# Performance work log

Measured on AMD Instinct MI355X. Metric: run time of the kernel, lower is better.

The kernel has to match this reference:

```python
import jax, jax.numpy as jnp
import numpy as np
from jax import lax

# dims (match init_kwargs)
NC, BS, H, W, OC, NT = 4, 16, 64, 64, 12, 32


def _conv(x, w):
    # NHWC 'same' 3x3 conv
    return lax.conv_general_dilated(x, w, (1, 1), 'SAME',
                                    dimension_numbers=('NHWC', 'HWIO', 'NHWC'))


def _convlstm_step(x, h, c, Wx, Wh, b):
    # Keras ConvLSTM2D, single timestep. Gate order i, f, g(c), o; activation=tanh,
    # recurrent_activation=hard_sigmoid.
    z = _conv(x, Wx) + _conv(h, Wh) + b
    i, f, g, o = jnp.split(z, 4, axis=-1)
    i = jax.nn.hard_sigmoid(i)
    f = jax.nn.hard_sigmoid(f)
    o = jax.nn.hard_sigmoid(o)
    c_new = f * c + i * jnp.tanh(g)
    h_new = o * jnp.tanh(c_new)
    return h_new, c_new


def setup_inputs() -> dict:
    key = jax.random.key(0)
    ks = jax.random.split(key, 8)
    sc = lambda k, shp: jax.random.normal(k, shp, jnp.float32) * 0.05
    return {
        'x': jax.random.normal(ks[0], (BS, NT, H, W, OC), jnp.float32),
        'class_ids': jax.random.randint(ks[1], (NT,), 0, NC),
        'Wx_g': sc(ks[2], (3, 3, NC * OC, 4 * OC)),  # general cell input kernel
        'Wh_g': sc(ks[3], (3, 3, OC, 4 * OC)),       # general cell recurrent kernel
        'b_g': jnp.zeros((4 * OC,), jnp.float32),
        'Wx_c': sc(ks[4], (3, 3, 2 * OC, 4 * OC)),   # class cell input kernel
        'Wh_c': sc(ks[5], (3, 3, OC, 4 * OC)),       # class cell recurrent kernel
        'b_c': jnp.zeros((4 * OC,), jnp.float32),
    }


def reference(x, class_ids, Wx_g, Wh_g, b_g, Wx_c, Wh_c, b_c):
    def step(carry, inp):
        class_h, class_c, gen_h, gen_c = carry
        frame, cid = inp
        # general cell reads the whole class-state bank (raw reshape, as in TF source)
        x_gen = jnp.reshape(class_h, (BS, H, W, NC * OC))
        gen_h, gen_c = _convlstm_step(x_gen, gen_h, gen_c, Wx_g, Wh_g, b_g)
        # class cell reads frame + fresh general representation
        aug = jnp.concatenate([frame, gen_h], axis=-1)  # (BS,H,W,2*OC)
        h_new, c_new = _convlstm_step(aug, class_h[cid], class_c[cid], Wx_c, Wh_c, b_c)
        # scatter update into class-indexed state banks
        class_h = class_h.at[cid].set(h_new)
        class_c = class_c.at[cid].set(c_new)
        return (class_h, class_c, gen_h, gen_c), h_new.reshape(BS, -1)

    z = jnp.zeros((NC, BS, H, W, OC), jnp.float32)
    g = jnp.zeros((BS, H, W, OC), jnp.float32)
    xs = (jnp.swapaxes(x, 0, 1), class_ids)  # time-major
    _, outs = lax.scan(step, (z, z, g, g), xs)
    # OuterLayer: sum over time of flattened per-step outputs
    return jnp.sum(outs, axis=0)  # (BS, H*W*OC)
```

## Files before the change

### kernel.cpp

```cpp
#include <hip/hip_runtime.h>
#include <hip/hip_bf16.h>

#define NCLS 4
#define BS   16
#define NT   32
#define OC   12
#define HW   4096
#define PIX  65536
#define STATE 786432
#define BANK  3145728

typedef short bf16x8 __attribute__((ext_vector_type(8)));
typedef float f32x4  __attribute__((ext_vector_type(4)));

__device__ __forceinline__ float hsig(float v){
    return fminf(fmaxf((v + 3.0f) * (1.0f/6.0f), 0.0f), 1.0f);
}
__device__ __forceinline__ short f2bf(float f){
    union { __hip_bfloat16 h; short s; } u;
    u.h = __float2bfloat16(f);
    return u.s;
}

__global__ __launch_bounds__(256) void repack_kernel(
    const float* __restrict__ Wxg, const float* __restrict__ Whg,
    const float* __restrict__ Wxc, const float* __restrict__ Whc,
    bf16x8* __restrict__ wgt)
{
    int id = blockIdx.x * 256 + threadIdx.x;
    if (id >= 6912) return;
    int cell = id / 3456;
    int rem  = id - cell * 3456;
    int tap  = rem / 384;  rem -= tap * 384;
    int kb   = rem / 192;  rem -= kb * 192;
    int nt   = rem / 64;
    int lane = rem - nt * 64;
    int quad = lane >> 4;
    int n    = nt * 16 + (lane & 15);
    union { bf16x8 v; short s[8]; } o;
    #pragma unroll
    for (int j = 0; j < 8; ++j){
        int k = kb * 32 + quad * 8 + j;
        float f = 0.0f;
        if (cell == 0){
            if (k < 48)      f = Wxg[(tap*48 + k)*48 + n];
            else if (k < 60) f = Whg[(tap*12 + (k-48))*48 + n];
        } else {
            if (k < 24)      f = Wxc[(tap*24 + k)*48 + n];
            else if (k < 36) f = Whc[(tap*12 + (k-24))*48 + n];
        }
        o.s[j] = f2bf(f);
    }
    wgt[id] = o.v;
}

__global__ __launch_bounds__(256) void convert_kernel(
    const float* __restrict__ x, short* __restrict__ xbf)
{
    int i = blockIdx.x * 256 + threadIdx.x;
    const float4* xf = (const float4*)x;
    float4 a = xf[i*2], b = xf[i*2 + 1];
    union { bf16x8 v; short s[8]; } o;
    o.s[0]=f2bf(a.x); o.s[1]=f2bf(a.y); o.s[2]=f2bf(a.z); o.s[3]=f2bf(a.w);
    o.s[4]=f2bf(b.x); o.s[5]=f2bf(b.y); o.s[6]=f2bf(b.z); o.s[7]=f2bf(b.w);
    ((bf16x8*)xbf)[i] = o.v;
}

#define HALO_SHORTS (8*198*8)

__device__ __forceinline__ int row_swizzle(int bid){
    return ((bid & 7) << 7) | (bid >> 3);
}

__global__ __launch_bounds__(256) void gen_kernel(
    short* __restrict__ bank,
    const short* __restrict__ hin,
    short* __restrict__ hout,
    float* __restrict__ cstate,
    const short* __restrict__ htmp_prev,
    const int* __restrict__ ids, int t,
    const bf16x8* __restrict__ wgt,
    const float* __restrict__ bias)
{
    __shared__ __align__(16) short halo[HALO_SHORTS];
    const int tid = threadIdx.x;
    const int rb  = row_swizzle(blockIdx.x);
    const int p0  = rb << 6;
    const int b   = p0 >> 12;
    const int y   = (p0 >> 6) & 63;

    const int cprev = (t > 0) ? ids[t-1] : -1;
    const bool slotmatch = (cprev >= 0) && ((b >> 2) == cprev);
    const short* bsrc = slotmatch ? htmp_prev : bank;

    for (int tk = tid; tk < 1584; tk += 256){
        int rc = tk >> 3, q8 = tk & 7;
        int r  = rc / 66, c = rc - r * 66;
        int yy = y + r - 1, xx = c - 1;
        bool valid = (yy >= 0) & (yy < 64) & (xx >= 0) & (xx < 64);
        int p  = (b << 12) + (yy << 6) + xx;
        int pb = slotmatch ? (p & 16383) : p;
        union { bf16x8 v; uint2 u2[2]; uint4 u4; } ch;
        ch.u4 = make_uint4(0u, 0u, 0u, 0u);
        if (valid){
            if (q8 < 6){
                ch.u4 = *(const uint4*)(bsrc + pb*48 + q8*8);
                if (slotmatch && r == 1)
                    *(uint4*)(bank + p*48 + q8*8) = ch.u4;
            } else if (q8 == 6){
                ch.u2[0] = *(const uint2*)(hin + p*12);
                ch.u2[1] = *(const uint2*)(hin + p*12 + 4);
            } else {
                ch.u2[0] = *(const uint2*)(hin + p*12 + 8);
            }
        }
        *(bf16x8*)&halo[(q8*198 + rc)*8] = ch.v;
    }
    __syncthreads();

    const int lane = tid & 63;
    const int w    = tid >> 6;
    const int m    = lane & 15;
    const int quad = lane >> 4;
    const int colbase = 16*w + m;

    f32x4 acc0 = {0.f,0.f,0.f,0.f};
    f32x4 acc1 = acc0, acc2 = acc0;
    #pragma unroll
    for (int ky = 0; ky < 3; ++ky){
        #pragma unroll
        for (int kx = 0; kx < 3; ++kx){
            const int tap = ky*3 + kx;
            #pragma unroll
            for (int kb = 0; kb < 2; ++kb){
                const bf16x8 a = *(const bf16x8*)
                    &halo[(((kb*4 + quad)*198) + ky*66 + colbase + kx)*8];
                const bf16x8* wp = wgt + ((tap*2 + kb)*3)*64 + lane;
                acc0 = __builtin_amdgcn_mfma_f32_16x16x32_bf16(a, wp[0],   acc0, 0,0,0);
                acc1 = __builtin_amdgcn_mfma_f32_16x16x32_bf16(a, wp[64],  acc1, 0,0,0);
                acc2 = __builtin_amdgcn_mfma_f32_16x16x32_bf16(a, wp[128], acc2, 0,0,0);
            }
        }
    }

    __syncthreads();
    float* zw = ((float*)halo) + w * 768;
    #pragma unroll
    for (int r = 0; r < 4; ++r){
        zw[(quad*4 + r)*48 +      m] = acc0[r];
        zw[(quad*4 + r)*48 + 16 + m] = acc1[r];
        zw[(quad*4 + r)*48 + 32 + m] = acc2[r];
    }
    __syncthreads();
    const int pbase = p0 + 16*w;
    #pragma unroll
    for (int s = 0; s < 3; ++s){
        int idx = lane*3 + s;
        int px  = idx / 12;
        int j   = idx - px*12;
        float zi = zw[px*48 +      j] + bias[j];
        float zf = zw[px*48 + 12 + j] + bias[12 + j];
        float zg = zw[px*48 + 24 + j] + bias[24 + j];
        float zo = zw[px*48 + 36 + j] + bias[36 + j];
        int off = pbase*12 + idx;
        float cold = cstate[off];
        float cn = hsig(zf)*cold + hsig(zi)*tanhf(zg);
        cstate[off] = cn;
        hout[off] = f2bf(hsig(zo)*tanhf(cn));
    }
}

__global__ __launch_bounds__(256) void class_kernel(
    const short* __restrict__ xbf,
    const int*   __restrict__ ids, int t,
    const short* __restrict__ ghn,
    const short* __restrict__ bank,
    float* __restrict__ class_c,
    const bf16x8* __restrict__ wgt,
    const float* __restrict__ bias,
    short* __restrict__ htmp,
    float* __restrict__ out)
{
    __shared__ __align__(16) short halo[HALO_SHORTS];
    const int tid = threadIdx.x;
    const int rb  = row_swizzle(blockIdx.x);
    const int p0  = rb << 6;
    const int b   = p0 >> 12;
    const int y   = (p0 >> 6) & 63;
    const int cid = ids[t];
    const short* chs   = bank + (size_t)cid * STATE;
    const short* frame = xbf + (size_t)(b*NT + t) * (HW*12);

    for (int tk = tid; tk < 1584; tk += 256){
        int rc = tk >> 3, q8 = tk & 7;
        int r  = rc / 66, c = rc - r * 66;
        int yy = y + r - 1, xx = c - 1;
        bool valid = (yy >= 0) & (yy < 64) & (xx >= 0) & (xx < 64);
        int pl = (yy << 6) + xx;
        int p  = (b << 12) + pl;
        union { bf16x8 v; uint2 u2[2]; uint4 u4; } ch;
        ch.u4 = make_uint4(0u, 0u, 0u, 0u);
        if (valid){
            if (q8 == 0){
                ch.u2[0] = *(const uint2*)(frame + pl*12);
                ch.u2[1] = *(const uint2*)(frame + pl*12 + 4);
            } else if (q8 == 1){
                ch.u2[0] = *(const uint2*)(frame + pl*12 + 8);
                ch.u2[1] = *(const uint2*)(ghn + p*12);
            } else if (q8 == 2){
                ch.u2[0] = *(const uint2*)(ghn + p*12 + 4);
                ch.u2[1] = *(const uint2*)(ghn + p*12 + 8);
            } else if (q8 == 3){
                ch.u2[0] = *(const uint2*)(chs + p*12);
                ch.u2[1] = *(const uint2*)(chs + p*12 + 4);
            } else if (q8 == 4){
                ch.u2[0] = *(const uint2*)(chs + p*12 + 8);
            }
        }
        *(bf16x8*)&halo[(q8*198 + rc)*8] = ch.v;
    }
    __syncthreads();

    const int lane = tid & 63;
    const int w    = tid >> 6;
    const int m    = lane & 15;
    const int quad = lane >> 4;
    const int colbase = 16*w + m;

    f32x4 acc0 = {0.f,0.f,0.f,0.f};
    f32x4 acc1 = acc0, acc2 = acc0;
    #pragma unroll
    for (int ky = 0; ky < 3; ++ky){
        #pragma unroll
        for (int kx = 0; kx < 3; ++kx){
            const int tap = ky*3 + kx;
            #pragma unroll
            for (int kb = 0; kb < 2; ++kb){
                const bf16x8 a = *(const bf16x8*)
                    &halo[(((kb*4 + quad)*198) + ky*66 + colbase + kx)*8];
                const bf16x8* wp = wgt + ((tap*2 + kb)*3)*64 + lane;
                acc0 = __builtin_amdgcn_mfma_f32_16x16x32_bf16(a, wp[0],   acc0, 0,0,0);
                acc1 = __builtin_amdgcn_mfma_f32_16x16x32_bf16(a, wp[64],  acc1, 0,0,0);
                acc2 = __builtin_amdgcn_mfma_f32_16x16x32_bf16(a, wp[128], acc2, 0,0,0);
            }
        }
    }

    __syncthreads();
    float* zw = ((float*)halo) + w * 768;
    #pragma unroll
    for (int r = 0; r < 4; ++r){
        zw[(quad*4 + r)*48 +      m] = acc0[r];
        zw[(quad*4 + r)*48 + 16 + m] = acc1[r];
        zw[(quad*4 + r)*48 + 32 + m] = acc2[r];
    }
    __syncthreads();
    float* cc = class_c + (size_t)cid * STATE;
    const int pbase = p0 + 16*w;
    #pragma unroll
    for (int s = 0; s < 3; ++s){
        int idx = lane*3 + s;
        int px  = idx / 12;
        int j   = idx - px*12;
        float zi = zw[px*48 +      j] + bias[j];
        float zf = zw[px*48 + 12 + j] + bias[12 + j];
        float zg = zw[px*48 + 24 + j] + bias[24 + j];
        float zo = zw[px*48 + 36 + j] + bias[36 + j];
        int off = pbase*12 + idx;
        float cold = cc[off];
        float cn = hsig(zf)*cold + hsig(zi)*tanhf(zg);
        cc[off] = cn;
        float h = hsig(zo)*tanhf(cn);
        htmp[off] = f2bf(h);
        out[off] += h;
    }
}

extern "C" void kernel_launch(void* const* d_in, const int* in_sizes, int n_in,
                              void* d_out, int out_size, void* d_ws, size_t ws_size,
                              hipStream_t stream)
{
    (void)in_sizes; (void)n_in; (void)out_size; (void)ws_size;
    const float* x    = (const float*)d_in[0];
    const int*   ids  = (const int*)  d_in[1];
    const float* Wxg  = (const float*)d_in[2];
    const float* Whg  = (const float*)d_in[3];
    const float* bg   = (const float*)d_in[4];
    const float* Wxc  = (const float*)d_in[5];
    const float* Whc  = (const float*)d_in[6];
    const float* bc   = (const float*)d_in[7];
    float* out = (float*)d_out;

    char* base = (char*)d_ws;
    short*  bank    = (short*) (base);
    float*  class_c = (float*) (base + 6291456);
    short*  genh0   = (short*) (base + 18874368);
    short*  genh1   = (short*) (base + 20447232);
    float*  gen_c   = (float*) (base + 22020096);
    short*  htmp0   = (short*) (base + 25165824);
    short*  htmp1   = (short*) (base + 26738688);
    short*  xbf     = (short*) (base + 28311552);
    bf16x8* wgt     = (bf16x8*)(base + 78643200);
    const bf16x8* wgt_gen = wgt;
    const bf16x8* wgt_cls = wgt + 3456;

    hipMemsetAsync(bank,    0, (size_t)2*BANK,  stream);
    hipMemsetAsync(class_c, 0, (size_t)4*BANK,  stream);
    hipMemsetAsync(genh0,   0, (size_t)2*STATE, stream);
    hipMemsetAsync(gen_c,   0, (size_t)4*STATE, stream);
    hipMemsetAsync(out,     0, (size_t)4*STATE, stream);

    repack_kernel<<<27, 256, 0, stream>>>(Wxg, Whg, Wxc, Whc, wgt);
    convert_kernel<<<12288, 256, 0, stream>>>(x, xbf);

    for (int t = 0; t < NT; ++t){
        short* hin       = (t & 1) ? genh1 : genh0;
        short* hnew      = (t & 1) ? genh0 : genh1;
        short* htmp_prev = (t & 1) ? htmp0 : htmp1;
        short* htmp_new  = (t & 1) ? htmp1 : htmp0;
        gen_kernel<<<1024, 256, 0, stream>>>(bank, hin, hnew, gen_c,
                                             htmp_prev, ids, t, wgt_gen, bg);
        class_kernel<<<1024, 256, 0, stream>>>(xbf, ids, t, hnew, bank, class_c,
                                               wgt_cls, bc, htmp_new, out);
    }
}
```

Measured before the change: 1.233 ms.

## Fuse input bf16 conversion into class kernel and restructure halo loads per pixel

Removes the separate convert_kernel that cast the whole fp32 input to bf16 up front. The class kernel now reads the fp32 frame directly and converts it while staging the halo. Both kernels now have one thread load every channel chunk of one halo pixel, replacing the old loop that spread chunks across threads. This drops a full-tensor read-write pass, but the per-step loads become wider fp32 reads and 58 of 256 threads sit idle during staging.

```diff
diff --git a/kernel.cpp b/kernel.cpp
--- a/kernel.cpp
+++ b/kernel.cpp
@@ -54,18 +54,6 @@
     wgt[id] = o.v;
 }
 
-__global__ __launch_bounds__(256) void convert_kernel(
-    const float* __restrict__ x, short* __restrict__ xbf)
-{
-    int i = blockIdx.x * 256 + threadIdx.x;
-    const float4* xf = (const float4*)x;
-    float4 a = xf[i*2], b = xf[i*2 + 1];
-    union { bf16x8 v; short s[8]; } o;
-    o.s[0]=f2bf(a.x); o.s[1]=f2bf(a.y); o.s[2]=f2bf(a.z); o.s[3]=f2bf(a.w);
-    o.s[4]=f2bf(b.x); o.s[5]=f2bf(b.y); o.s[6]=f2bf(b.z); o.s[7]=f2bf(b.w);
-    ((bf16x8*)xbf)[i] = o.v;
-}
-
 #define HALO_SHORTS (8*198*8)
 
 __device__ __forceinline__ int row_swizzle(int bid){
@@ -93,28 +81,41 @@
     const bool slotmatch = (cprev >= 0) && ((b >> 2) == cprev);
     const short* bsrc = slotmatch ? htmp_prev : bank;
 
-    for (int tk = tid; tk < 1584; tk += 256){
-        int rc = tk >> 3, q8 = tk & 7;
-        int r  = rc / 66, c = rc - r * 66;
+    {
+        const int i = tid;
+        const bool active = (i < 198);
+        int r  = i / 66, c = i - r * 66;
         int yy = y + r - 1, xx = c - 1;
-        bool valid = (yy >= 0) & (yy < 64) & (xx >= 0) & (xx < 64);
+        bool valid = active & (yy >= 0) & (yy < 64) & (xx >= 0) & (xx < 64);
         int p  = (b << 12) + (yy << 6) + xx;
         int pb = slotmatch ? (p & 16383) : p;
-        union { bf16x8 v; uint2 u2[2]; uint4 u4; } ch;
-        ch.u4 = make_uint4(0u, 0u, 0u, 0u);
+        uint4 bk[6]; uint2 h0, h1, h2;
+        #pragma unroll
+        for (int q = 0; q < 6; ++q) bk[q] = make_uint4(0u,0u,0u,0u);
+        h0 = make_uint2(0u,0u); h1 = h0; h2 = h0;
         if (valid){
-            if (q8 < 6){
-                ch.u4 = *(const uint4*)(bsrc + pb*48 + q8*8);
-                if (slotmatch && r == 1)
-                    *(uint4*)(bank + p*48 + q8*8) = ch.u4;
-            } else if (q8 == 6){
-                ch.u2[0] = *(const uint2*)(hin + p*12);
-                ch.u2[1] = *(const uint2*)(hin + p*12 + 4);
-            } else {
-                ch.u2[0] = *(const uint2*)(hin + p*12 + 8);
+            const short* bp = bsrc + pb*48;
+            #pragma unroll
+            for (int q = 0; q < 6; ++q) bk[q] = *(const uint4*)(bp + q*8);
+            h0 = *(const uint2*)(hin + p*12);
+            h1 = *(const uint2*)(hin + p*12 + 4);
+            h2 = *(const uint2*)(hin + p*12 + 8);
+            if (slotmatch && r == 1){
+                #pragma unroll
+                for (int q = 0; q < 6; ++q)
+                    *(uint4*)(bank + p*48 + q*8) = bk[q];
             }
         }
-        *(bf16x8*)&halo[(q8*198 + rc)*8] = ch.v;
+        if (active){
+            #pragma unroll
+            for (int q = 0; q < 6; ++q)
+                *(uint4*)&halo[(q*198 + i)*8] = bk[q];
+            union { uint2 u2[2]; uint4 u4; } p6, p7;
+            p6.u2[0] = h0; p6.u2[1] = h1;
+            p7.u2[0] = h2; p7.u2[1] = make_uint2(0u,0u);
+            *(uint4*)&halo[(6*198 + i)*8] = p6.u4;
+            *(uint4*)&halo[(7*198 + i)*8] = p7.u4;
+        }
     }
     __syncthreads();
 
@@ -171,7 +172,7 @@
 }
 
 __global__ __launch_bounds__(256) void class_kernel(
-    const short* __restrict__ xbf,
+    const float* __restrict__ xall,
     const int*   __restrict__ ids, int t,
     const short* __restrict__ ghn,
     const short* __restrict__ bank,
@@ -189,35 +190,50 @@
     const int y   = (p0 >> 6) & 63;
     const int cid = ids[t];
     const short* chs   = bank + (size_t)cid * STATE;
-    const short* frame = xbf + (size_t)(b*NT + t) * (HW*12);
-
-    for (int tk = tid; tk < 1584; tk += 256){
-        int rc = tk >> 3, q8 = tk & 7;
-        int r  = rc / 66, c = rc - r * 66;
+    const float* frame = xall + (size_t)(b*NT + t) * (HW*12);
+
+    {
+        const int i = tid;
+        const bool active = (i < 198);
+        int r  = i / 66, c = i - r * 66;
         int yy = y + r - 1, xx = c - 1;
-        bool valid = (yy >= 0) & (yy < 64) & (xx >= 0) & (xx < 64);
+        bool valid = active & (yy >= 0) & (yy < 64) & (xx >= 0) & (xx < 64);
         int pl = (yy << 6) + xx;
         int p  = (b << 12) + pl;
-        union { bf16x8 v; uint2 u2[2]; uint4 u4; } ch;
-        ch.u4 = make_uint4(0u, 0u, 0u, 0u);
+        float4 f0, f1, f2;
+        f0 = make_float4(0.f,0.f,0.f,0.f); f1 = f0; f2 = f0;
+        uint2 g0, g1, g2, s0, s1, s2;
+        g0 = make_uint2(0u,0u); g1 = g0; g2 = g0; s0 = g0; s1 = g0; s2 = g0;
         if (valid){
-            if (q8 == 0){
-                ch.u2[0] = *(const uint2*)(frame + pl*12);
-                ch.u2[1] = *(const uint2*)(frame + pl*12 + 4);
-            } else if (q8 == 1){
-                ch.u2[0] = *(const uint2*)(frame + pl*12 + 8);
-                ch.u2[1] = *(const uint2*)(ghn + p*12);
-            } else if (q8 == 2){
-                ch.u2[0] = *(const uint2*)(ghn + p*12 + 4);
-                ch.u2[1] = *(const uint2*)(ghn + p*12 + 8);
-            } else if (q8 == 3){
-                ch.u2[0] = *(const uint2*)(chs + p*12);
-                ch.u2[1] = *(const uint2*)(chs + p*12 + 4);
-            } else if (q8 == 4){
-                ch.u2[0] = *(const uint2*)(chs + p*12 + 8);
-            }
-        }
-        *(bf16x8*)&halo[(q8*198 + rc)*8] = ch.v;
+            f0 = *(const float4*)(frame + pl*12);
+            f1 = *(const float4*)(frame + pl*12 + 4);
+            f2 = *(const float4*)(frame + pl*12 + 8);
+            g0 = *(const uint2*)(ghn + p*12);
+            g1 = *(const uint2*)(ghn + p*12 + 4);
+            g2 = *(const uint2*)(ghn + p*12 + 8);
+            s0 = *(const uint2*)(chs + p*12);
+            s1 = *(const uint2*)(chs + p*12 + 4);
+            s2 = *(const uint2*)(chs + p*12 + 8);
+        }
+        if (active){
+            union { uint4 u4; uint2 u2[2]; short s[8]; } pk;
+            pk.s[0]=f2bf(f0.x); pk.s[1]=f2bf(f0.y); pk.s[2]=f2bf(f0.z); pk.s[3]=f2bf(f0.w);
+            pk.s[4]=f2bf(f1.x); pk.s[5]=f2bf(f1.y); pk.s[6]=f2bf(f1.z); pk.s[7]=f2bf(f1.w);
+            *(uint4*)&halo[(0*198 + i)*8] = pk.u4;
+            pk.s[0]=f2bf(f2.x); pk.s[1]=f2bf(f2.y); pk.s[2]=f2bf(f2.z); pk.s[3]=f2bf(f2.w);
+            pk.u2[1] = g0;
+            *(uint4*)&halo[(1*198 + i)*8] = pk.u4;
+            pk.u2[0] = g1; pk.u2[1] = g2;
+            *(uint4*)&halo[(2*198 + i)*8] = pk.u4;
+            pk.u2[0] = s0; pk.u2[1] = s1;
+            *(uint4*)&halo[(3*198 + i)*8] = pk.u4;
+            pk.u2[0] = s2; pk.u2[1] = make_uint2(0u,0u);
+            *(uint4*)&halo[(4*198 + i)*8] = pk.u4;
+            uint4 z = make_uint4(0u,0u,0u,0u);
+            *(uint4*)&halo[(5*198 + i)*8] = z;
+            *(uint4*)&halo[(6*198 + i)*8] = z;
+            *(uint4*)&halo[(7*198 + i)*8] = z;
+        }
     }
     __syncthreads();
 
@@ -299,8 +315,7 @@
     float*  gen_c   = (float*) (base + 22020096);
     short*  htmp0   = (short*) (base + 25165824);
     short*  htmp1   = (short*) (base + 26738688);
-    short*  xbf     = (short*) (base + 28311552);
-    bf16x8* wgt     = (bf16x8*)(base + 78643200);
+    bf16x8* wgt     = (bf16x8*)(base + 28311552);
     const bf16x8* wgt_gen = wgt;
     const bf16x8* wgt_cls = wgt + 3456;
 
@@ -311,7 +326,6 @@
     hipMemsetAsync(out,     0, (size_t)4*STATE, stream);
 
     repack_kernel<<<27, 256, 0, stream>>>(Wxg, Whg, Wxc, Whc, wgt);
-    convert_kernel<<<12288, 256, 0, stream>>>(x, xbf);
 
     for (int t = 0; t < NT; ++t){
         short* hin       = (t & 1) ? genh1 : genh0;
@@ -320,7 +334,7 @@
         short* htmp_new  = (t & 1) ? htmp1 : htmp0;
         gen_kernel<<<1024, 256, 0, stream>>>(bank, hin, hnew, gen_c,
                                              htmp_prev, ids, t, wgt_gen, bg);
-        class_kernel<<<1024, 256, 0, stream>>>(xbf, ids, t, hnew, bank, class_c,
+        class_kernel<<<1024, 256, 0, stream>>>(x, ids, t, hnew, bank, class_c,
                                                wgt_cls, bc, htmp_new, out);
     }
 }
```

Result: faster. 1.069 ms (-13.3%).
